# Optimization experiments

Hardware: AMD Instinct MI355X
Metric: run time of the kernel (lower is better)

## Reference

```python
import jax, jax.numpy as jnp
import numpy as np

# ESN dims: reservoir R, input I, output O, timesteps T
R, I, O, T = 4096, 64, 64, 8192
SPECTRAL_RADIUS = 0.9


def setup_inputs() -> dict:
    key = jax.random.key(0)
    k1, k2, k3, k4 = jax.random.split(key, 4)
    X = jax.random.normal(k1, (T, I), jnp.float32)
    W_in = jax.random.normal(k2, (R, I), jnp.float32) / np.float32(np.sqrt(I))
    # scale recurrent matrix so its spectral radius is ~SPECTRAL_RADIUS
    W_res = jax.random.normal(k3, (R, R), jnp.float32) * np.float32(SPECTRAL_RADIUS / np.sqrt(R))
    W_out = jax.random.normal(k4, (O, I + R), jnp.float32) / np.float32(np.sqrt(I + R))
    return {"X": X, "W_in": W_in, "W_res": W_res, "W_out": W_out}


def reference(X, W_in, W_res, W_out):
    """BatchESN.predict: sequential reservoir recurrence + linear readout.

    state_{t} = tanh(W_in @ x_t + W_res @ state_{t-1})
    y_t       = W_out @ concat(x_t, state_t)
    """
    reservoir = W_res.shape[0]

    def step(state, x):
        new_state = jnp.tanh(W_in @ x + W_res @ state)
        out = W_out @ jnp.concatenate([x, new_state])  # [O]
        return new_state, out

    state0 = jnp.zeros((reservoir,), dtype=X.dtype)
    _, preds = jax.lax.scan(step, state0, X)  # preds: [T, O]
    return preds
```

## Files before the change

kernel.cpp:

```cpp
#include <hip/hip_runtime.h>
#include <math.h>

#define R_DIM 4096
#define I_DIM 64
#define O_DIM 64
#define T_DIM 8192
#define NBLK  256
#define NTHR  512
#define RPB   16
#define LROWS 8

#define LBAR() asm volatile("s_waitcnt lgkmcnt(0)\n\ts_barrier" ::: "memory")


__global__ __launch_bounds__(NTHR, 2) void esn_persist(
    const float* __restrict__ X, const float* __restrict__ Wres,
    const float* __restrict__ Win, const float* __restrict__ Wout,
    float* __restrict__ out, unsigned long long* __restrict__ pairs,
    float* __restrict__ Shist, int use_hist)
{
    __shared__ __align__(16) float wlds[LROWS * R_DIM];
    __shared__ __align__(16) float sdata[R_DIM + I_DIM];
    __shared__ float4 red4[8];

    const int tid  = threadIdx.x;
    const int b    = blockIdx.x;
    const int lane = tid & 63;
    const int w    = tid >> 6;
    const int rg   = tid >> 7;
    const int cg   = tid & 127;
    const int R0   = b * RPB;

    const int rm0 = 2 * rg, rm1 = 2 * rg + 1;

    {
        const float4* wsrc = (const float4*)(Wres + (size_t)R0 * R_DIM);
        float4* wdst = (float4*)wlds;
#pragma unroll
        for (int k = 0; k < (LROWS * R_DIM / 4) / NTHR; ++k)
            wdst[k * NTHR + tid] = wsrc[k * NTHR + tid];
    }
    float4 wreg[2][8];
#pragma unroll
    for (int rr = 0; rr < 2; ++rr) {
        const float* rowp = Wres + (size_t)(R0 + 8 + 2 * rg + rr) * R_DIM + cg * 4;
#pragma unroll
        for (int i = 0; i < 8; ++i)
            wreg[rr][i] = *(const float4*)(rowp + i * 512);
    }
#pragma unroll
    for (int rr = 0; rr < 2; ++rr)
#pragma unroll
        for (int i = 0; i < 8; ++i)
            asm volatile("" : "+v"(wreg[rr][i].x), "+v"(wreg[rr][i].y),
                             "+v"(wreg[rr][i].z), "+v"(wreg[rr][i].w));

    float4 wi[4] = {};
    if (cg < 16) {
        wi[0] = *(const float4*)(Win + (size_t)(R0 + rm0) * I_DIM + cg * 4);
        wi[1] = *(const float4*)(Win + (size_t)(R0 + rm1) * I_DIM + cg * 4);
        wi[2] = *(const float4*)(Win + (size_t)(R0 + 8 + 2 * rg) * I_DIM + cg * 4);
        wi[3] = *(const float4*)(Win + (size_t)(R0 + 9 + 2 * rg) * I_DIM + cg * 4);
    }
    float4 wo4[4] = {};
    if (!use_hist && w == 1) {
#pragma unroll
        for (int j = 0; j < 4; ++j)
            wo4[j] = *(const float4*)(Wout + (size_t)lane * (I_DIM + R_DIM) + I_DIM + R0 + j * 4);
    }

    for (int t = 0; t < T_DIM; ++t) {
        if (tid < I_DIM) sdata[R_DIM + tid] = X[(size_t)t * I_DIM + tid];
        {
            unsigned long long* rbuf = pairs + ((t + 1) & 1) * R_DIM;
            const int base = w * 512 + lane;
            const unsigned tagmin = (unsigned)t;
            float vals[8];
            unsigned got = 0;
            while (got != 0xFFu) {
#pragma unroll
                for (int k = 0; k < 8; ++k) {
                    if (!(got & (1u << k))) {
                        unsigned long long p = __hip_atomic_load(&rbuf[base + k * 64],
                                              __ATOMIC_RELAXED, __HIP_MEMORY_SCOPE_AGENT);
                        if ((unsigned)(p >> 32) >= tagmin) {
                            vals[k] = __uint_as_float((unsigned)p);
                            got |= 1u << k;
                        }
                    }
                }
                if (got != 0xFFu) __builtin_amdgcn_s_sleep(1);
            }
#pragma unroll
            for (int k = 0; k < 8; ++k) sdata[base + k * 64] = vals[k];
        }
        LBAR();

        float acc0 = 0.f, acc1 = 0.f, acc2 = 0.f, acc3 = 0.f;
#pragma unroll
        for (int i = 0; i < 8; ++i) {
            const int col = cg * 4 + i * 512;
            float4 sv = *(const float4*)&sdata[col];
            float4 l0 = *(const float4*)&wlds[rm0 * R_DIM + col];
            float4 l1 = *(const float4*)&wlds[rm1 * R_DIM + col];
            acc0 += l0.x * sv.x + l0.y * sv.y + l0.z * sv.z + l0.w * sv.w;
            acc1 += l1.x * sv.x + l1.y * sv.y + l1.z * sv.z + l1.w * sv.w;
            acc2 += wreg[0][i].x * sv.x + wreg[0][i].y * sv.y + wreg[0][i].z * sv.z + wreg[0][i].w * sv.w;
            acc3 += wreg[1][i].x * sv.x + wreg[1][i].y * sv.y + wreg[1][i].z * sv.z + wreg[1][i].w * sv.w;
        }
        if (cg < 16) {
            float4 xv = *(const float4*)&sdata[R_DIM + cg * 4];
            acc0 += wi[0].x * xv.x + wi[0].y * xv.y + wi[0].z * xv.z + wi[0].w * xv.w;
            acc1 += wi[1].x * xv.x + wi[1].y * xv.y + wi[1].z * xv.z + wi[1].w * xv.w;
            acc2 += wi[2].x * xv.x + wi[2].y * xv.y + wi[2].z * xv.z + wi[2].w * xv.w;
            acc3 += wi[3].x * xv.x + wi[3].y * xv.y + wi[3].z * xv.z + wi[3].w * xv.w;
        }
#pragma unroll
        for (int d = 1; d < 64; d <<= 1) {
            acc0 += __shfl_xor(acc0, d);
            acc1 += __shfl_xor(acc1, d);
            acc2 += __shfl_xor(acc2, d);
            acc3 += __shfl_xor(acc3, d);
        }
        if (lane == 0) red4[w] = make_float4(acc0, acc1, acc2, acc3);
        LBAR();

        if (w == 0) {
            asm volatile("s_waitcnt vmcnt(0)" ::: "memory");
            if (lane < RPB) {
                const int rgp = lane >> 2, rr = lane & 3;
                const int row = (rr < 2) ? (2 * rgp + rr) : (6 + 2 * rgp + rr);
                float pre = ((const float*)&red4[rgp * 2])[rr] + ((const float*)&red4[rgp * 2 + 1])[rr];
                float s = tanhf(pre);
                unsigned long long p = ((unsigned long long)(unsigned)(t + 1) << 32)
                                     | (unsigned long long)__float_as_uint(s);
                __hip_atomic_store(&pairs[(t & 1) * R_DIM + R0 + row], p,
                                   __ATOMIC_RELAXED, __HIP_MEMORY_SCOPE_AGENT);
                if (use_hist) Shist[(size_t)t * R_DIM + R0 + row] = s;
            }
        } else if (w == 1 && !use_hist) {
            float s = 0.f;
            if (lane < RPB) {
                const int rgp = lane >> 2, rr = lane & 3;
                float pre = ((const float*)&red4[rgp * 2])[rr] + ((const float*)&red4[rgp * 2 + 1])[rr];
                s = tanhf(pre);
            }
            float y = 0.f;
#pragma unroll
            for (int j = 0; j < 16; ++j) {
                const int src = (j < 8) ? ((j >> 1) * 4 + (j & 1))
                                        : (((j - 8) >> 1) * 4 + 2 + ((j - 8) & 1));
                float sj = __shfl(s, src);
                y += ((const float*)wo4)[j] * sj;
            }
            __hip_atomic_fetch_add(&out[(size_t)t * O_DIM + lane], y,
                                   __ATOMIC_RELAXED, __HIP_MEMORY_SCOPE_AGENT);
        }
        if (!use_hist) LBAR();
    }
}

__global__ void esn_xpart(const float* __restrict__ X, const float* __restrict__ Wout,
                          float* __restrict__ out)
{
    const int idx = blockIdx.x * blockDim.x + threadIdx.x;
    const int t = idx >> 6, o = idx & 63;
    const float4* xr = (const float4*)(X + (size_t)t * I_DIM);
    const float4* wr = (const float4*)(Wout + (size_t)o * (I_DIM + R_DIM));
    float y = 0.f;
#pragma unroll
    for (int j = 0; j < 16; ++j) {
        float4 a = xr[j], b = wr[j];
        y += a.x * b.x + a.y * b.y + a.z * b.z + a.w * b.w;
    }
    out[idx] = y;
}

__global__ void esn_readout(const float* __restrict__ Shist, const float* __restrict__ Wout,
                            float* __restrict__ out)
{
    const int idx = blockIdx.x * blockDim.x + threadIdx.x;
    const int t = idx >> 6, o = idx & 63;
    const float4* s4 = (const float4*)(Shist + (size_t)t * R_DIM);
    const float4* w4 = (const float4*)(Wout + (size_t)o * (I_DIM + R_DIM) + I_DIM);
    float y = 0.f;
#pragma unroll 4
    for (int j = 0; j < R_DIM / 4; ++j) {
        float4 a = s4[j], b = w4[j];
        y += a.x * b.x + a.y * b.y + a.z * b.z + a.w * b.w;
    }
    out[idx] += y;
}

extern "C" void kernel_launch(void* const* d_in, const int* in_sizes, int n_in,
                              void* d_out, int out_size, void* d_ws, size_t ws_size,
                              hipStream_t stream)
{
    (void)in_sizes; (void)n_in; (void)out_size;
    const float* X    = (const float*)d_in[0];
    const float* Win  = (const float*)d_in[1];
    const float* Wres = (const float*)d_in[2];
    const float* Wout = (const float*)d_in[3];
    float* out = (float*)d_out;

    unsigned long long* pairs = (unsigned long long*)d_ws;
    float* Shist = (float*)((char*)d_ws + 65536);
    const size_t hist_bytes = (size_t)T_DIM * R_DIM * sizeof(float);
    const int use_hist = (ws_size >= 65536 + hist_bytes) ? 1 : 0;

    hipMemsetAsync(d_ws, 0, 65536, stream);

    esn_xpart<<<(T_DIM * O_DIM) / 256, 256, 0, stream>>>(X, Wout, out);

    void* args[] = { (void*)&X, (void*)&Wres, (void*)&Win, (void*)&Wout,
                     (void*)&out, (void*)&pairs, (void*)&Shist, (void*)&use_hist };
    hipLaunchCooperativeKernel((const void*)esn_persist, dim3(NBLK), dim3(NTHR),
                               args, 0, stream);

    if (use_hist)
        esn_readout<<<(T_DIM * O_DIM) / 256, 256, 0, stream>>>(Shist, Wout, out);
}
```

Baseline: 38.96 ms.

## Replace tagged state pairs with per-block flags and plain state buffer

Each block now publishes its step count in a per-block flag after storing its 16 state values to a double-buffered float array. Consumers poll 256 flags (4 per thread, wave-wide vote) and then bulk-load the previous state as 64-bit words, instead of polling 4096 tagged 64-bit pairs with per-element retries. This is meant to cut global polling traffic and halve the bytes moved per state exchange. It adds a flag-after-data ordering that relies on relaxed atomics plus vmcnt waits rather than explicit release/acquire fences, which may not be strictly guaranteed across CUs.

```diff
diff --git a/kernel.cpp b/kernel.cpp
--- a/kernel.cpp
+++ b/kernel.cpp
@@ -16,8 +16,8 @@
 __global__ __launch_bounds__(NTHR, 2) void esn_persist(
     const float* __restrict__ X, const float* __restrict__ Wres,
     const float* __restrict__ Win, const float* __restrict__ Wout,
-    float* __restrict__ out, unsigned long long* __restrict__ pairs,
-    float* __restrict__ Shist, int use_hist)
+    float* __restrict__ out, unsigned* __restrict__ flags,
+    float* __restrict__ S, float* __restrict__ Shist, int use_hist)
 {
     __shared__ __align__(16) float wlds[LROWS * R_DIM];
     __shared__ __align__(16) float sdata[R_DIM + I_DIM];
@@ -69,30 +69,37 @@
             wo4[j] = *(const float4*)(Wout + (size_t)lane * (I_DIM + R_DIM) + I_DIM + R0 + j * 4);
     }
 
+    const int f0 = tid >> 3;
+
     for (int t = 0; t < T_DIM; ++t) {
-        if (tid < I_DIM) sdata[R_DIM + tid] = X[(size_t)t * I_DIM + tid];
+        float xval = 0.f;
+        if (tid < I_DIM) xval = X[(size_t)t * I_DIM + tid];
+
+        if (t) {
+            const unsigned tgt = (unsigned)t;
+            while (1) {
+                unsigned a = __hip_atomic_load(&flags[f0      ], __ATOMIC_RELAXED, __HIP_MEMORY_SCOPE_AGENT);
+                unsigned c = __hip_atomic_load(&flags[f0 + 64 ], __ATOMIC_RELAXED, __HIP_MEMORY_SCOPE_AGENT);
+                unsigned d = __hip_atomic_load(&flags[f0 + 128], __ATOMIC_RELAXED, __HIP_MEMORY_SCOPE_AGENT);
+                unsigned e = __hip_atomic_load(&flags[f0 + 192], __ATOMIC_RELAXED, __HIP_MEMORY_SCOPE_AGENT);
+                if (__all(a >= tgt && c >= tgt && d >= tgt && e >= tgt)) break;
+                __builtin_amdgcn_s_sleep(1);
+            }
+        }
+
         {
-            unsigned long long* rbuf = pairs + ((t + 1) & 1) * R_DIM;
-            const int base = w * 512 + lane;
-            const unsigned tagmin = (unsigned)t;
-            float vals[8];
-            unsigned got = 0;
-            while (got != 0xFFu) {
-#pragma unroll
-                for (int k = 0; k < 8; ++k) {
-                    if (!(got & (1u << k))) {
-                        unsigned long long p = __hip_atomic_load(&rbuf[base + k * 64],
-                                              __ATOMIC_RELAXED, __HIP_MEMORY_SCOPE_AGENT);
-                        if ((unsigned)(p >> 32) >= tagmin) {
-                            vals[k] = __uint_as_float((unsigned)p);
-                            got |= 1u << k;
-                        }
-                    }
-                }
-                if (got != 0xFFu) __builtin_amdgcn_s_sleep(1);
-            }
-#pragma unroll
-            for (int k = 0; k < 8; ++k) sdata[base + k * 64] = vals[k];
+            const unsigned long long* sprev =
+                (const unsigned long long*)(S + ((t + 1) & 1) * R_DIM);
+            unsigned long long v0 = __hip_atomic_load(&sprev[tid           ], __ATOMIC_RELAXED, __HIP_MEMORY_SCOPE_AGENT);
+            unsigned long long v1 = __hip_atomic_load(&sprev[tid + 1 * NTHR], __ATOMIC_RELAXED, __HIP_MEMORY_SCOPE_AGENT);
+            unsigned long long v2 = __hip_atomic_load(&sprev[tid + 2 * NTHR], __ATOMIC_RELAXED, __HIP_MEMORY_SCOPE_AGENT);
+            unsigned long long v3 = __hip_atomic_load(&sprev[tid + 3 * NTHR], __ATOMIC_RELAXED, __HIP_MEMORY_SCOPE_AGENT);
+            unsigned long long* dst = (unsigned long long*)sdata;
+            dst[tid           ] = v0;
+            dst[tid + 1 * NTHR] = v1;
+            dst[tid + 2 * NTHR] = v2;
+            dst[tid + 3 * NTHR] = v3;
+            if (tid < I_DIM) sdata[R_DIM + tid] = xval;
         }
         LBAR();
 
@@ -126,18 +133,19 @@
         LBAR();
 
         if (w == 0) {
-            asm volatile("s_waitcnt vmcnt(0)" ::: "memory");
             if (lane < RPB) {
                 const int rgp = lane >> 2, rr = lane & 3;
                 const int row = (rr < 2) ? (2 * rgp + rr) : (6 + 2 * rgp + rr);
                 float pre = ((const float*)&red4[rgp * 2])[rr] + ((const float*)&red4[rgp * 2 + 1])[rr];
                 float s = tanhf(pre);
-                unsigned long long p = ((unsigned long long)(unsigned)(t + 1) << 32)
-                                     | (unsigned long long)__float_as_uint(s);
-                __hip_atomic_store(&pairs[(t & 1) * R_DIM + R0 + row], p,
+                __hip_atomic_store(&S[(t & 1) * R_DIM + R0 + row], s,
                                    __ATOMIC_RELAXED, __HIP_MEMORY_SCOPE_AGENT);
                 if (use_hist) Shist[(size_t)t * R_DIM + R0 + row] = s;
             }
+            asm volatile("s_waitcnt vmcnt(0)" ::: "memory");
+            if (lane == 0)
+                __hip_atomic_store(&flags[b], (unsigned)(t + 1),
+                                   __ATOMIC_RELAXED, __HIP_MEMORY_SCOPE_AGENT);
         } else if (w == 1 && !use_hist) {
             float s = 0.f;
             if (lane < RPB) {
@@ -203,17 +211,18 @@
     const float* Wout = (const float*)d_in[3];
     float* out = (float*)d_out;
 
-    unsigned long long* pairs = (unsigned long long*)d_ws;
+    unsigned* flags = (unsigned*)d_ws;
+    float* S     = (float*)((char*)d_ws + 1024);
     float* Shist = (float*)((char*)d_ws + 65536);
     const size_t hist_bytes = (size_t)T_DIM * R_DIM * sizeof(float);
     const int use_hist = (ws_size >= 65536 + hist_bytes) ? 1 : 0;
 
-    hipMemsetAsync(d_ws, 0, 65536, stream);
+    hipMemsetAsync(d_ws, 0, 1024 + 2 * R_DIM * sizeof(float), stream);
 
     esn_xpart<<<(T_DIM * O_DIM) / 256, 256, 0, stream>>>(X, Wout, out);
 
     void* args[] = { (void*)&X, (void*)&Wres, (void*)&Win, (void*)&Wout,
-                     (void*)&out, (void*)&pairs, (void*)&Shist, (void*)&use_hist };
+                     (void*)&out, (void*)&flags, (void*)&S, (void*)&Shist, (void*)&use_hist };
     hipLaunchCooperativeKernel((const void*)esn_persist, dim3(NBLK), dim3(NTHR),
                                args, 0, stream);
 
```

Result: slower. 49.02 ms (+25.8%).

## Pack exchanged reservoir state as fp16 with 16-bit tag, rebalance LDS/register rows

Applied to the files above, without the earlier changes.

Each step's cross-block state exchange now writes one 32-bit word (16-bit step tag plus the fp16 state value) instead of a 64-bit tag/fp32 pair. This halves the polled and stored bytes per element and lets the poll use 32-bit atomics. The sleep in the spin loop is removed so waiting blocks poll continuously. The W_res rows per block are redistributed: 4 rows now sit in LDS and 12 in registers (3 per row group), which frees shared memory. The cost is raised register pressure, which risks spills at this launch bound, and the recurrence now feeds fp16-rounded state, which can reduce accuracy over 8192 steps.

```diff
diff --git a/kernel.cpp b/kernel.cpp
--- a/kernel.cpp
+++ b/kernel.cpp
@@ -1,4 +1,5 @@
 #include <hip/hip_runtime.h>
+#include <hip/hip_fp16.h>
 #include <math.h>
 
 #define R_DIM 4096
@@ -8,7 +9,7 @@
 #define NBLK  256
 #define NTHR  512
 #define RPB   16
-#define LROWS 8
+#define LROWS 4
 
 #define LBAR() asm volatile("s_waitcnt lgkmcnt(0)\n\ts_barrier" ::: "memory")
 
@@ -16,7 +17,7 @@
 __global__ __launch_bounds__(NTHR, 2) void esn_persist(
     const float* __restrict__ X, const float* __restrict__ Wres,
     const float* __restrict__ Win, const float* __restrict__ Wout,
-    float* __restrict__ out, unsigned long long* __restrict__ pairs,
+    float* __restrict__ out, unsigned* __restrict__ pairs,
     float* __restrict__ Shist, int use_hist)
 {
     __shared__ __align__(16) float wlds[LROWS * R_DIM];
@@ -31,8 +32,6 @@
     const int cg   = tid & 127;
     const int R0   = b * RPB;
 
-    const int rm0 = 2 * rg, rm1 = 2 * rg + 1;
-
     {
         const float4* wsrc = (const float4*)(Wres + (size_t)R0 * R_DIM);
         float4* wdst = (float4*)wlds;
@@ -40,16 +39,16 @@
         for (int k = 0; k < (LROWS * R_DIM / 4) / NTHR; ++k)
             wdst[k * NTHR + tid] = wsrc[k * NTHR + tid];
     }
-    float4 wreg[2][8];
-#pragma unroll
-    for (int rr = 0; rr < 2; ++rr) {
-        const float* rowp = Wres + (size_t)(R0 + 8 + 2 * rg + rr) * R_DIM + cg * 4;
+    float4 wreg[3][8];
+#pragma unroll
+    for (int rr = 0; rr < 3; ++rr) {
+        const float* rowp = Wres + (size_t)(R0 + 4 + 3 * rg + rr) * R_DIM + cg * 4;
 #pragma unroll
         for (int i = 0; i < 8; ++i)
             wreg[rr][i] = *(const float4*)(rowp + i * 512);
     }
 #pragma unroll
-    for (int rr = 0; rr < 2; ++rr)
+    for (int rr = 0; rr < 3; ++rr)
 #pragma unroll
         for (int i = 0; i < 8; ++i)
             asm volatile("" : "+v"(wreg[rr][i].x), "+v"(wreg[rr][i].y),
@@ -57,10 +56,10 @@
 
     float4 wi[4] = {};
     if (cg < 16) {
-        wi[0] = *(const float4*)(Win + (size_t)(R0 + rm0) * I_DIM + cg * 4);
-        wi[1] = *(const float4*)(Win + (size_t)(R0 + rm1) * I_DIM + cg * 4);
-        wi[2] = *(const float4*)(Win + (size_t)(R0 + 8 + 2 * rg) * I_DIM + cg * 4);
-        wi[3] = *(const float4*)(Win + (size_t)(R0 + 9 + 2 * rg) * I_DIM + cg * 4);
+        wi[0] = *(const float4*)(Win + (size_t)(R0 + rg) * I_DIM + cg * 4);
+        wi[1] = *(const float4*)(Win + (size_t)(R0 + 4 + 3 * rg) * I_DIM + cg * 4);
+        wi[2] = *(const float4*)(Win + (size_t)(R0 + 5 + 3 * rg) * I_DIM + cg * 4);
+        wi[3] = *(const float4*)(Win + (size_t)(R0 + 6 + 3 * rg) * I_DIM + cg * 4);
     }
     float4 wo4[4] = {};
     if (!use_hist && w == 1) {
@@ -72,7 +71,7 @@
     for (int t = 0; t < T_DIM; ++t) {
         if (tid < I_DIM) sdata[R_DIM + tid] = X[(size_t)t * I_DIM + tid];
         {
-            unsigned long long* rbuf = pairs + ((t + 1) & 1) * R_DIM;
+            unsigned* rbuf = pairs + ((t + 1) & 1) * R_DIM;
             const int base = w * 512 + lane;
             const unsigned tagmin = (unsigned)t;
             float vals[8];
@@ -81,15 +80,14 @@
 #pragma unroll
                 for (int k = 0; k < 8; ++k) {
                     if (!(got & (1u << k))) {
-                        unsigned long long p = __hip_atomic_load(&rbuf[base + k * 64],
-                                              __ATOMIC_RELAXED, __HIP_MEMORY_SCOPE_AGENT);
-                        if ((unsigned)(p >> 32) >= tagmin) {
-                            vals[k] = __uint_as_float((unsigned)p);
+                        unsigned p = __hip_atomic_load(&rbuf[base + k * 64],
+                                      __ATOMIC_RELAXED, __HIP_MEMORY_SCOPE_AGENT);
+                        if ((p >> 16) >= tagmin) {
+                            vals[k] = __half2float(__ushort_as_half((unsigned short)(p & 0xFFFFu)));
                             got |= 1u << k;
                         }
                     }
                 }
-                if (got != 0xFFu) __builtin_amdgcn_s_sleep(1);
             }
 #pragma unroll
             for (int k = 0; k < 8; ++k) sdata[base + k * 64] = vals[k];
@@ -101,12 +99,11 @@
         for (int i = 0; i < 8; ++i) {
             const int col = cg * 4 + i * 512;
             float4 sv = *(const float4*)&sdata[col];
-            float4 l0 = *(const float4*)&wlds[rm0 * R_DIM + col];
-            float4 l1 = *(const float4*)&wlds[rm1 * R_DIM + col];
+            float4 l0 = *(const float4*)&wlds[rg * R_DIM + col];
             acc0 += l0.x * sv.x + l0.y * sv.y + l0.z * sv.z + l0.w * sv.w;
-            acc1 += l1.x * sv.x + l1.y * sv.y + l1.z * sv.z + l1.w * sv.w;
-            acc2 += wreg[0][i].x * sv.x + wreg[0][i].y * sv.y + wreg[0][i].z * sv.z + wreg[0][i].w * sv.w;
-            acc3 += wreg[1][i].x * sv.x + wreg[1][i].y * sv.y + wreg[1][i].z * sv.z + wreg[1][i].w * sv.w;
+            acc1 += wreg[0][i].x * sv.x + wreg[0][i].y * sv.y + wreg[0][i].z * sv.z + wreg[0][i].w * sv.w;
+            acc2 += wreg[1][i].x * sv.x + wreg[1][i].y * sv.y + wreg[1][i].z * sv.z + wreg[1][i].w * sv.w;
+            acc3 += wreg[2][i].x * sv.x + wreg[2][i].y * sv.y + wreg[2][i].z * sv.z + wreg[2][i].w * sv.w;
         }
         if (cg < 16) {
             float4 xv = *(const float4*)&sdata[R_DIM + cg * 4];
@@ -129,12 +126,12 @@
             asm volatile("s_waitcnt vmcnt(0)" ::: "memory");
             if (lane < RPB) {
                 const int rgp = lane >> 2, rr = lane & 3;
-                const int row = (rr < 2) ? (2 * rgp + rr) : (6 + 2 * rgp + rr);
+                const int row = (rr == 0) ? rgp : (4 + 3 * rgp + (rr - 1));
                 float pre = ((const float*)&red4[rgp * 2])[rr] + ((const float*)&red4[rgp * 2 + 1])[rr];
                 float s = tanhf(pre);
-                unsigned long long p = ((unsigned long long)(unsigned)(t + 1) << 32)
-                                     | (unsigned long long)__float_as_uint(s);
-                __hip_atomic_store(&pairs[(t & 1) * R_DIM + R0 + row], p,
+                unsigned pack = ((unsigned)(t + 1) << 16)
+                              | (unsigned)__half_as_ushort(__float2half(s));
+                __hip_atomic_store(&pairs[(t & 1) * R_DIM + R0 + row], pack,
                                    __ATOMIC_RELAXED, __HIP_MEMORY_SCOPE_AGENT);
                 if (use_hist) Shist[(size_t)t * R_DIM + R0 + row] = s;
             }
@@ -148,8 +145,8 @@
             float y = 0.f;
 #pragma unroll
             for (int j = 0; j < 16; ++j) {
-                const int src = (j < 8) ? ((j >> 1) * 4 + (j & 1))
-                                        : (((j - 8) >> 1) * 4 + 2 + ((j - 8) & 1));
+                const int src = (j < 4) ? (4 * j)
+                                        : (4 * ((j - 4) / 3) + ((j - 4) % 3) + 1);
                 float sj = __shfl(s, src);
                 y += ((const float*)wo4)[j] * sj;
             }
@@ -203,12 +200,12 @@
     const float* Wout = (const float*)d_in[3];
     float* out = (float*)d_out;
 
-    unsigned long long* pairs = (unsigned long long*)d_ws;
+    unsigned* pairs = (unsigned*)d_ws;
     float* Shist = (float*)((char*)d_ws + 65536);
     const size_t hist_bytes = (size_t)T_DIM * R_DIM * sizeof(float);
     const int use_hist = (ws_size >= 65536 + hist_bytes) ? 1 : 0;
 
-    hipMemsetAsync(d_ws, 0, 65536, stream);
+    hipMemsetAsync(d_ws, 0, 2 * R_DIM * sizeof(unsigned), stream);
 
     esn_xpart<<<(T_DIM * O_DIM) / 256, 256, 0, stream>>>(X, Wout, out);
 
```

Result: faster. 37.04 ms (-4.9%).
